# Kernel optimization log

Measured on AMD Instinct MI355X. Metric: run time of the kernel, lower is better.

Reference implementation:

```python
import jax, jax.numpy as jnp
import numpy as np

DT = 0.05
DX = 1.0
NUM_STEPS = 3
EPS = 1e-6
MAX_COEFF = 1.0  # use_implicit=True


def _thomas_const(r, d, eps):
    """Batched Thomas solve for the constant-coefficient system used by the ADI
    sweeps: off-diagonals a=c=-r, diagonal 1+2r with Neumann-like ends 1+r.
    Faithful to the torch solver including the +eps on b[0] and the
    clamp(min=eps) on interior denominators. d: (M, n) -> (M, n)."""
    n = d.shape[-1]
    a = -r  # scalar (lower == upper == -r)
    b = jnp.full((n,), 1.0 + 2.0 * r, dtype=d.dtype).at[0].set(1.0 + r).at[-1].set(1.0 + r)
    # forward elimination for c' and denominators (scalar per position)
    cp0 = a / (b[0] + eps)
    def fwd_c(cp_prev, bi):
        denom = jnp.maximum(bi - a * cp_prev, eps)
        cp = a / denom
        return cp, (cp, denom)
    _, (cps, denoms) = jax.lax.scan(fwd_c, cp0, b[1:])
    cp = jnp.concatenate([cp0[None], cps]).at[-1].set(0.0)  # (n,); last entry unused (torch leaves it 0)
    # forward sweep for d' over the whole batch of RHS vectors
    dT = jnp.moveaxis(d, -1, 0)  # (n, M)
    dp0 = dT[0] / (b[0] + eps)
    def fwd_d(dp_prev, xs):
        di, denom = xs
        dp = (di - a * dp_prev) / denom
        return dp, dp
    _, dps = jax.lax.scan(fwd_d, dp0, (dT[1:], denoms))
    dp = jnp.concatenate([dp0[None], dps], axis=0)  # (n, M)
    # back substitution
    xn = dp[-1]
    def back(x_next, xs):
        dpi, cpi = xs
        x = dpi - cpi * x_next
        return x, x
    _, xs_ = jax.lax.scan(back, xn, (dp[:-1], cp[:-1]), reverse=True)
    x = jnp.concatenate([xs_, xn[None]], axis=0)  # (n, M)
    return jnp.moveaxis(x, 0, -1)


def _forward(u, alpha_base, beta_base, alpha_spatial, beta_spatial, channel_coupling):
    B, C, H, W = u.shape
    # torch.einsum('cc,bci->bci', coupling, u) multiplies by the DIAGONAL of coupling
    diag = jnp.diagonal(channel_coupling)  # (C,)
    for step in range(NUM_STEPS):
        t = step * DT
        alpha_t = jnp.clip(alpha_base + alpha_spatial.mean(axis=(1, 2)) * t, EPS, MAX_COEFF)  # (C,)
        beta_t = jnp.clip(beta_base + beta_spatial.mean(axis=(1, 2)) * t, EPS, MAX_COEFF)
        r_a = alpha_t * (DT / 2.0) / DX ** 2  # ADI half-steps
        r_b = beta_t * (DT / 2.0) / DX ** 2
        uc = jnp.moveaxis(u, 1, 0)  # (C, B, H, W); coefficients differ per channel
        solve_x = lambda r, d: _thomas_const(r, d.reshape(B * H, W), EPS).reshape(B, H, W)
        ux = jax.vmap(solve_x)(r_a, uc)
        solve_y = lambda r, d: jnp.swapaxes(
            _thomas_const(r, jnp.swapaxes(d, 1, 2).reshape(B * W, H), EPS).reshape(B, W, H), 1, 2)
        uy = jax.vmap(solve_y)(r_b, ux)
        u = jnp.moveaxis(uy, 0, 1) * diag[None, :, None, None]
    return u


def setup_inputs() -> dict:
    key = jax.random.key(0)
    k = jax.random.split(key, 6)
    B, C, S = 128, 3, 256
    u = jax.random.normal(k[0], (B, C, S, S), dtype=jnp.float32)
    alpha_base = 0.3 + 0.01 * jax.random.normal(k[1], (C,), dtype=jnp.float32)
    beta_base = 0.3 + 0.01 * jax.random.normal(k[2], (C,), dtype=jnp.float32)
    alpha_spatial = 0.01 * jax.random.normal(k[3], (C, S, S), dtype=jnp.float32)
    beta_spatial = 0.01 * jax.random.normal(k[4], (C, S, S), dtype=jnp.float32)
    channel_coupling = 0.05 * jnp.eye(C, dtype=jnp.float32) + 0.01 * jax.random.normal(k[5], (C, C), dtype=jnp.float32)
    return {"u": u, "alpha_base": alpha_base, "beta_base": beta_base,
            "alpha_spatial": alpha_spatial, "beta_spatial": beta_spatial,
            "channel_coupling": channel_coupling}


def reference(u, alpha_base, beta_base, alpha_spatial, beta_spatial, channel_coupling):
    return _forward(u, alpha_base, beta_base, alpha_spatial, beta_spatial, channel_coupling)
```

## Files before the change

kernel.cpp:

```cpp
#include <hip/hip_runtime.h>

constexpr int Bn = 128, Cn = 3, Sn = 256;
constexpr int HWn = Sn * Sn;
constexpr int NPLANE = Bn * Cn;
constexpr float DTf = 0.05f;
constexpr float EPSf = 1e-6f;
constexpr float MAXCf = 1.0f;

#define WS_TAPX 128
#define WS_TAPY 10368

__global__ void build_taps(const float* __restrict__ alpha_base,
                           const float* __restrict__ beta_base,
                           const float* __restrict__ aspat,
                           const float* __restrict__ bspat,
                           const float* __restrict__ coupling,
                           float* __restrict__ ws) {
  __shared__ double sm[256];
  __shared__ float cp3[3][288], di3[3][288];
  __shared__ float s_mean;
  const int dirc = blockIdx.x, dir = dirc / 3, c = dirc % 3;
  const int j = threadIdx.x;
  {
    const float4* p = (const float4*)((dir == 0 ? aspat : bspat) + c * HWn) + j;
    double acc = 0.0;
#pragma unroll
    for (int k2 = 0; k2 < 64; ++k2) {
      float4 v = p[k2 * 256];
      acc += (double)v.x + (double)v.y + (double)v.z + (double)v.w;
    }
    sm[j] = acc;
    __syncthreads();
    for (int s2 = 128; s2 > 0; s2 >>= 1) {
      if (j < s2) sm[j] += sm[j + s2];
      __syncthreads();
    }
    if (j == 0) s_mean = (float)(sm[0] * (1.0 / 65536.0));
    __syncthreads();
  }
  if (j < 3) {
    const int k = j;
    const float base = (dir == 0) ? alpha_base[c] : beta_base[c];
    const float coef = fminf(fmaxf(base + s_mean * ((float)k * DTf), EPSf), MAXCf);
    const float r = coef * (DTf * 0.5f);
    for (int p = 0; p < 16; ++p) {
      cp3[k][p] = 0.f; di3[k][p] = 0.f;
      cp3[k][272 + p] = 0.f; di3[k][272 + p] = 0.f;
    }
    float b0 = 1.f + r + EPSf;
    float cq = -r / b0, dq = 1.f / b0;
    cp3[k][16] = cq; di3[k][16] = dq;
    for (int i = 1; i < 256; ++i) {
      float b = (i == 255) ? (1.f + r) : (1.f + 2.f * r);
      float den = fmaxf(b + r * cq, EPSf);
      cq = -r / den; dq = 1.f / den;
      cp3[k][16 + i] = cq; di3[k][16 + i] = dq;
    }
  }
  float* tb = ws + ((dir == 0) ? WS_TAPX : WS_TAPY) + c * 13 * 256;
#pragma unroll
  for (int d = 0; d < 13; ++d) tb[d * 256 + j] = 0.f;
  __syncthreads();

  float z[33];
#pragma unroll
  for (int o = 0; o < 33; ++o) z[o] = (o == 16) ? 1.f : 0.f;
#pragma unroll
  for (int k = 0; k < 3; ++k) {
    float dp = 0.f;
#pragma unroll
    for (int o = 0; o < 33; ++o) {
      const int p = j + o;
      dp = fmaf(-cp3[k][p], dp, z[o] * di3[k][p]);
      z[o] = dp;
    }
    float x = 0.f;
#pragma unroll
    for (int o = 32; o >= 0; --o) {
      const int p = j + o;
      x = fmaf(-cp3[k][p], x, z[o]);
      z[o] = x;
    }
  }
  float scale = 1.f;
  if (dir == 1) {
    float dgc = coupling[c * 3 + c];
    scale = dgc * dgc * dgc;
  }
#pragma unroll
  for (int o = -6; o <= 6; ++o) {
    const int i = j + o;
    if ((unsigned)i < 256u) tb[(6 - o) * 256 + i] = z[o + 16] * scale;
  }
}

__global__ __launch_bounds__(512, 4) void conv3(
    const float* __restrict__ src, float* __restrict__ dst,
    const float* __restrict__ ws) {
  __shared__ float vt[76 * 256];
  const int t = threadIdx.x;
  const int logical = (blockIdx.x & 7) * 192 + (blockIdx.x >> 3);
  const int plane = logical >> 2;
  const int st = logical & 3;
  const int c = plane % 3;
  const int h0 = st * 64;
  const int a = (st == 0) ? 0 : (h0 - 6);
  const int b = (st == 3) ? 256 : (h0 + 70);
  const int Wv = b - a;
  const float* tpx = ws + WS_TAPX + c * 3328;
  const float* tpy = ws + WS_TAPY + c * 3328;
  const float* srcp = src + (size_t)plane * HWn;

  {
    const int wv = t >> 6, l = t & 63;
    const int fl = l ^ (l >> 3);
#pragma unroll
    for (int m = 0; m < 3; ++m) {
#pragma unroll
      for (int jj = 0; jj < 4; ++jj) {
        const int rl = 4 * wv + jj + 32 * m;
        if (rl < Wv) {
          const float* gp = srcp + (size_t)(a + rl) * 256 + (fl << 2);
          __builtin_amdgcn_global_load_lds(
              (const __attribute__((address_space(1))) void*)gp,
              (__attribute__((address_space(3))) void*)(vt + rl * 256), 16, 0, 0);
        }
      }
    }
  }
  float tx[13];
#pragma unroll
  for (int d = 0; d < 13; ++d) tx[d] = tpx[d * 256 + 128];
  asm volatile("s_waitcnt vmcnt(0)" ::: "memory");
  __builtin_amdgcn_sched_barrier(0);

  const int NU = 16 * Wv;
#pragma unroll
  for (int p = 0; p < 3; ++p) {
    const int u = t + 512 * p;
    if (u < NU) {
      const int s = u & 15, rl = u >> 4;
      float* base = vt + rl * 256;
      float in_[32];
#pragma unroll
      for (int mq = 0; mq < 8; ++mq) {
        int g = 4 * s - 2 + mq;
        g = g < 0 ? 0 : (g > 63 ? 63 : g);
        const int sl = g ^ (g >> 3);
        *(float4*)&in_[4 * mq] = *(const float4*)(base + 4 * sl);
      }
      float acc[16];
#pragma unroll
      for (int e = 0; e < 16; ++e) acc[e] = tx[0] * in_[e + 2];
#pragma unroll
      for (int d = 1; d < 13; ++d)
#pragma unroll
        for (int e = 0; e < 16; ++e) acc[e] = fmaf(tx[d], in_[e + 2 + d], acc[e]);
      if (s == 0) {
#pragma unroll
        for (int e = 0; e < 6; ++e) {
          float ac = 0.f;
#pragma unroll
          for (int d = 0; d < 13; ++d) ac = fmaf(tpx[d * 256 + e], in_[e + 2 + d], ac);
          acc[e] = ac;
        }
      } else if (s == 15) {
#pragma unroll
        for (int e = 10; e < 16; ++e) {
          float ac = 0.f;
#pragma unroll
          for (int d = 0; d < 13; ++d) ac = fmaf(tpx[d * 256 + 240 + e], in_[e + 2 + d], ac);
          acc[e] = ac;
        }
      }
#pragma unroll
      for (int jj = 0; jj < 4; ++jj) {
        const int q = 4 * s + jj;
        const int sl = q ^ (q >> 3);
        *(float4*)(base + 4 * sl) =
            make_float4(acc[4 * jj], acc[4 * jj + 1], acc[4 * jj + 2], acc[4 * jj + 3]);
      }
    }
  }
  __syncthreads();

  const int pr = t & 127, rc = t >> 7;
  const int jq = pr >> 1;
  const int wpos = ((jq ^ (jq >> 3)) << 2) | ((pr & 1) * 2);
  const int g0 = h0 + 16 * rc;
  float2 win[13];
#pragma unroll
  for (int m = 0; m < 12; ++m) {
    int gg = g0 - 6 + m;
    gg = gg < a ? a : gg;
    win[m] = *(const float2*)(vt + (gg - a) * 256 + wpos);
  }
  float* dstp = dst + (size_t)plane * HWn + 2 * pr;
#pragma unroll
  for (int rr = 0; rr < 16; ++rr) {
    const int g = g0 + rr;
    {
      int gg = g + 6;
      gg = gg > b - 1 ? b - 1 : gg;
      win[12] = *(const float2*)(vt + (gg - a) * 256 + wpos);
    }
    const int gu = __builtin_amdgcn_readfirstlane(g);
    float ox, oy;
    {
      const float ty = tpy[gu];
      ox = ty * win[0].x; oy = ty * win[0].y;
    }
#pragma unroll
    for (int d = 1; d < 13; ++d) {
      const float ty = tpy[d * 256 + gu];
      ox = fmaf(ty, win[d].x, ox);
      oy = fmaf(ty, win[d].y, oy);
    }
    *(float2*)(dstp + (size_t)g * 256) = make_float2(ox, oy);
#pragma unroll
    for (int m = 0; m < 12; ++m) win[m] = win[m + 1];
  }
}

extern "C" void kernel_launch(void* const* d_in, const int* in_sizes, int n_in,
                              void* d_out, int out_size, void* d_ws, size_t ws_size,
                              hipStream_t stream) {
  const float* u = (const float*)d_in[0];
  const float* alpha_base = (const float*)d_in[1];
  const float* beta_base = (const float*)d_in[2];
  const float* alpha_spatial = (const float*)d_in[3];
  const float* beta_spatial = (const float*)d_in[4];
  const float* coupling = (const float*)d_in[5];
  float* out = (float*)d_out;
  float* ws = (float*)d_ws;

  build_taps<<<6, 256, 0, stream>>>(alpha_base, beta_base,
                                    alpha_spatial, beta_spatial, coupling, ws);
  conv3<<<NPLANE * 4, 512, 0, stream>>>(u, out, ws);
}
```

Before: 90.69 us.

## Stream row chunks through small LDS ring buffer pipelining x and y stencils

Replaces the load-all-then-compute conv kernel with an 11-iteration loop. Each iteration loads 8 rows into a small staging buffer, applies the x-direction stencil into a 32-row ring buffer, and computes y-direction outputs from earlier rows. The aim is to cut LDS use from 76 rows to 40 so occupancy can rise (launch bounds 4→6) and to overlap global loads with compute. In exchange it adds two barriers per iteration, a full vmcnt wait each step, and padded rows whose float4 accesses may be misaligned.

```diff
diff --git a/kernel.cpp b/kernel.cpp
--- a/kernel.cpp
+++ b/kernel.cpp
@@ -94,131 +94,120 @@
   }
 }
 
-__global__ __launch_bounds__(512, 4) void conv3(
+__global__ __launch_bounds__(512, 6) void conv_pipe(
     const float* __restrict__ src, float* __restrict__ dst,
     const float* __restrict__ ws) {
-  __shared__ float vt[76 * 256];
+  __shared__ float Vb[32 * 266];
+  __shared__ float Ub[8 * 266];
   const int t = threadIdx.x;
   const int logical = (blockIdx.x & 7) * 192 + (blockIdx.x >> 3);
   const int plane = logical >> 2;
-  const int st = logical & 3;
+  const int R = logical & 3;
   const int c = plane % 3;
-  const int h0 = st * 64;
-  const int a = (st == 0) ? 0 : (h0 - 6);
-  const int b = (st == 3) ? 256 : (h0 + 70);
-  const int Wv = b - a;
   const float* tpx = ws + WS_TAPX + c * 3328;
   const float* tpy = ws + WS_TAPY + c * 3328;
   const float* srcp = src + (size_t)plane * HWn;
-
-  {
-    const int wv = t >> 6, l = t & 63;
-    const int fl = l ^ (l >> 3);
-#pragma unroll
-    for (int m = 0; m < 3; ++m) {
-#pragma unroll
-      for (int jj = 0; jj < 4; ++jj) {
-        const int rl = 4 * wv + jj + 32 * m;
-        if (rl < Wv) {
-          const float* gp = srcp + (size_t)(a + rl) * 256 + (fl << 2);
-          __builtin_amdgcn_global_load_lds(
-              (const __attribute__((address_space(1))) void*)gp,
-              (__attribute__((address_space(3))) void*)(vt + rl * 256), 16, 0, 0);
+  float* dstp = dst + (size_t)plane * HWn;
+  const int g_base = 64 * R - 6;
+
+  float tx[13];
+#pragma unroll
+  for (int d = 0; d < 13; ++d) tx[d] = tpx[d * 256 + 128];
+
+  const int xs = t >> 3, xr = t & 7;
+  const int yp = t & 127, ysub = t >> 7;
+  const int wv = t >> 6, l = t & 63;
+
+  for (int i = 0; i < 11; ++i) {
+    if (i < 10) {
+      const int r = 8 * i + wv;
+      if (r < 76) {
+        int G = g_base + r;
+        G = G < 0 ? 0 : (G > 255 ? 255 : G);
+        const float* gp = srcp + (size_t)G * 256 + 4 * l;
+        __builtin_amdgcn_global_load_lds(
+            (const __attribute__((address_space(1))) void*)gp,
+            (__attribute__((address_space(3))) void*)(Ub + wv * 266), 16, 0, 0);
+      }
+    }
+    if (i >= 3) {
+      const int j = i - 3;
+      const int r0 = 6 + 8 * j + 2 * ysub;
+      const int g0 = g_base + r0;
+      float2 win[14];
+#pragma unroll
+      for (int d = 0; d < 14; ++d) {
+        const int slot = (r0 - 6 + d) & 31;
+        win[d] = *(const float2*)(Vb + slot * 266 + 2 * yp);
+      }
+      const int gu = __builtin_amdgcn_readfirstlane(g0);
+      float ox0, oy0, ox1, oy1;
+      {
+        const float ty0 = tpy[gu];
+        ox0 = ty0 * win[0].x; oy0 = ty0 * win[0].y;
+        const float ty1 = tpy[gu + 1];
+        ox1 = ty1 * win[1].x; oy1 = ty1 * win[1].y;
+      }
+#pragma unroll
+      for (int d = 1; d < 13; ++d) {
+        const float ty0 = tpy[d * 256 + gu];
+        ox0 = fmaf(ty0, win[d].x, ox0); oy0 = fmaf(ty0, win[d].y, oy0);
+        const float ty1 = tpy[d * 256 + gu + 1];
+        ox1 = fmaf(ty1, win[d + 1].x, ox1); oy1 = fmaf(ty1, win[d + 1].y, oy1);
+      }
+      *(float2*)(dstp + (size_t)g0 * 256 + 2 * yp) = make_float2(ox0, oy0);
+      *(float2*)(dstp + (size_t)(g0 + 1) * 256 + 2 * yp) = make_float2(ox1, oy1);
+    }
+    asm volatile("s_waitcnt vmcnt(0)" ::: "memory");
+    __syncthreads();
+    if (i < 10) {
+      const int r = 8 * i + xr;
+      if (r < 76) {
+        float in_[16];
+#pragma unroll
+        for (int m = 0; m < 8; ++m) {
+          int cp = 4 * xs - 6 + 2 * m;
+          cp = cp < 0 ? 0 : (cp > 254 ? 254 : cp);
+          *(float2*)&in_[2 * m] = *(const float2*)(Ub + xr * 266 + cp);
         }
-      }
-    }
-  }
-  float tx[13];
-#pragma unroll
-  for (int d = 0; d < 13; ++d) tx[d] = tpx[d * 256 + 128];
-  asm volatile("s_waitcnt vmcnt(0)" ::: "memory");
-  __builtin_amdgcn_sched_barrier(0);
-
-  const int NU = 16 * Wv;
-#pragma unroll
-  for (int p = 0; p < 3; ++p) {
-    const int u = t + 512 * p;
-    if (u < NU) {
-      const int s = u & 15, rl = u >> 4;
-      float* base = vt + rl * 256;
-      float in_[32];
-#pragma unroll
-      for (int mq = 0; mq < 8; ++mq) {
-        int g = 4 * s - 2 + mq;
-        g = g < 0 ? 0 : (g > 63 ? 63 : g);
-        const int sl = g ^ (g >> 3);
-        *(float4*)&in_[4 * mq] = *(const float4*)(base + 4 * sl);
-      }
-      float acc[16];
-#pragma unroll
-      for (int e = 0; e < 16; ++e) acc[e] = tx[0] * in_[e + 2];
-#pragma unroll
-      for (int d = 1; d < 13; ++d)
-#pragma unroll
-        for (int e = 0; e < 16; ++e) acc[e] = fmaf(tx[d], in_[e + 2 + d], acc[e]);
-      if (s == 0) {
-#pragma unroll
-        for (int e = 0; e < 6; ++e) {
-          float ac = 0.f;
-#pragma unroll
-          for (int d = 0; d < 13; ++d) ac = fmaf(tpx[d * 256 + e], in_[e + 2 + d], ac);
-          acc[e] = ac;
+        float acc[4];
+#pragma unroll
+        for (int e = 0; e < 4; ++e) acc[e] = tx[0] * in_[e];
+#pragma unroll
+        for (int d = 1; d < 13; ++d)
+#pragma unroll
+          for (int e = 0; e < 4; ++e) acc[e] = fmaf(tx[d], in_[e + d], acc[e]);
+        if (xs < 2) {
+#pragma unroll
+          for (int e = 0; e < 4; ++e) {
+            const int col = 4 * xs + e;
+            if (col < 6) {
+              float a = 0.f;
+#pragma unroll
+              for (int d = 0; d < 13; ++d)
+                a = fmaf(tpx[d * 256 + col], in_[e + d], a);
+              acc[e] = a;
+            }
+          }
+        } else if (xs >= 62) {
+#pragma unroll
+          for (int e = 0; e < 4; ++e) {
+            const int col = 4 * xs + e;
+            if (col >= 250) {
+              float a = 0.f;
+#pragma unroll
+              for (int d = 0; d < 13; ++d)
+                a = fmaf(tpx[d * 256 + col], in_[e + d], a);
+              acc[e] = a;
+            }
+          }
         }
-      } else if (s == 15) {
-#pragma unroll
-        for (int e = 10; e < 16; ++e) {
-          float ac = 0.f;
-#pragma unroll
-          for (int d = 0; d < 13; ++d) ac = fmaf(tpx[d * 256 + 240 + e], in_[e + 2 + d], ac);
-          acc[e] = ac;
-        }
-      }
-#pragma unroll
-      for (int jj = 0; jj < 4; ++jj) {
-        const int q = 4 * s + jj;
-        const int sl = q ^ (q >> 3);
-        *(float4*)(base + 4 * sl) =
-            make_float4(acc[4 * jj], acc[4 * jj + 1], acc[4 * jj + 2], acc[4 * jj + 3]);
-      }
-    }
-  }
-  __syncthreads();
-
-  const int pr = t & 127, rc = t >> 7;
-  const int jq = pr >> 1;
-  const int wpos = ((jq ^ (jq >> 3)) << 2) | ((pr & 1) * 2);
-  const int g0 = h0 + 16 * rc;
-  float2 win[13];
-#pragma unroll
-  for (int m = 0; m < 12; ++m) {
-    int gg = g0 - 6 + m;
-    gg = gg < a ? a : gg;
-    win[m] = *(const float2*)(vt + (gg - a) * 256 + wpos);
-  }
-  float* dstp = dst + (size_t)plane * HWn + 2 * pr;
-#pragma unroll
-  for (int rr = 0; rr < 16; ++rr) {
-    const int g = g0 + rr;
-    {
-      int gg = g + 6;
-      gg = gg > b - 1 ? b - 1 : gg;
-      win[12] = *(const float2*)(vt + (gg - a) * 256 + wpos);
-    }
-    const int gu = __builtin_amdgcn_readfirstlane(g);
-    float ox, oy;
-    {
-      const float ty = tpy[gu];
-      ox = ty * win[0].x; oy = ty * win[0].y;
-    }
-#pragma unroll
-    for (int d = 1; d < 13; ++d) {
-      const float ty = tpy[d * 256 + gu];
-      ox = fmaf(ty, win[d].x, ox);
-      oy = fmaf(ty, win[d].y, oy);
-    }
-    *(float2*)(dstp + (size_t)g * 256) = make_float2(ox, oy);
-#pragma unroll
-    for (int m = 0; m < 12; ++m) win[m] = win[m + 1];
+        const int slot = r & 31;
+        *(float4*)(Vb + slot * 266 + 4 * xs) =
+            make_float4(acc[0], acc[1], acc[2], acc[3]);
+      }
+    }
+    __syncthreads();
   }
 }
 
@@ -236,5 +225,5 @@
 
   build_taps<<<6, 256, 0, stream>>>(alpha_base, beta_base,
                                     alpha_spatial, beta_spatial, coupling, ws);
-  conv3<<<NPLANE * 4, 512, 0, stream>>>(u, out, ws);
+  conv_pipe<<<NPLANE * 4, 512, 0, stream>>>(u, out, ws);
 }
```

Measured after the change: 238.9 us. 163% more time.

## Split fused separable convolution into separate x and y kernels via workspace

Applied to the files above, without the earlier changes.

Replaces the single fused conv3 kernel with two kernels: convx applies the horizontal 13-tap filter row-wise and writes to a full-size workspace buffer, and convy applies the vertical filter from that buffer. This removes the halo recomputation and large LDS footprint of the fused tile but adds a full extra write and read of the 100MB intermediate. The fallback conv3 now reads global memory directly instead of using async LDS loads, and uses a different LDS swizzle. Which path runs depends on the workspace size.

```diff
diff --git a/kernel.cpp b/kernel.cpp
--- a/kernel.cpp
+++ b/kernel.cpp
@@ -9,6 +9,7 @@
 
 #define WS_TAPX 128
 #define WS_TAPY 10368
+#define WS_TMP  20480
 
 __global__ void build_taps(const float* __restrict__ alpha_base,
                            const float* __restrict__ beta_base,
@@ -91,6 +92,101 @@
   for (int o = -6; o <= 6; ++o) {
     const int i = j + o;
     if ((unsigned)i < 256u) tb[(6 - o) * 256 + i] = z[o + 16] * scale;
+  }
+}
+
+__global__ __launch_bounds__(256, 4) void convx(
+    const float* __restrict__ src, float* __restrict__ tmp,
+    const float* __restrict__ ws) {
+  const int t = threadIdx.x;
+  const int rid = blockIdx.x * 16 + (t >> 4);
+  const int s = t & 15;
+  const int c = (rid >> 8) % 3;
+  const float* tpx = ws + WS_TAPX + c * 3328;
+  float tx[13];
+#pragma unroll
+  for (int d = 0; d < 13; ++d) tx[d] = tpx[d * 256 + 128];
+  const float* row = src + (size_t)rid * 256;
+  float in_[32];
+#pragma unroll
+  for (int mq = 0; mq < 8; ++mq) {
+    int cl = 16 * s - 8 + 4 * mq;
+    cl = cl < 0 ? 0 : (cl > 252 ? 252 : cl);
+    *(float4*)&in_[4 * mq] = *(const float4*)(row + cl);
+  }
+  float acc[16];
+#pragma unroll
+  for (int e = 0; e < 16; ++e) acc[e] = tx[0] * in_[e + 2];
+#pragma unroll
+  for (int d = 1; d < 13; ++d)
+#pragma unroll
+    for (int e = 0; e < 16; ++e) acc[e] = fmaf(tx[d], in_[e + 2 + d], acc[e]);
+  if (s == 0) {
+#pragma unroll
+    for (int e = 0; e < 6; ++e) {
+      float ac = 0.f;
+#pragma unroll
+      for (int d = 0; d < 13; ++d) ac = fmaf(tpx[d * 256 + e], in_[e + 2 + d], ac);
+      acc[e] = ac;
+    }
+  } else if (s == 15) {
+#pragma unroll
+    for (int e = 10; e < 16; ++e) {
+      float ac = 0.f;
+#pragma unroll
+      for (int d = 0; d < 13; ++d) ac = fmaf(tpx[d * 256 + 240 + e], in_[e + 2 + d], ac);
+      acc[e] = ac;
+    }
+  }
+  float* op = tmp + (size_t)rid * 256 + 16 * s;
+#pragma unroll
+  for (int jj = 0; jj < 4; ++jj)
+    *(float4*)(op + 4 * jj) =
+        make_float4(acc[4 * jj], acc[4 * jj + 1], acc[4 * jj + 2], acc[4 * jj + 3]);
+}
+
+__global__ __launch_bounds__(256, 4) void convy(
+    const float* __restrict__ tmp, float* __restrict__ dst,
+    const float* __restrict__ ws) {
+  const int t = threadIdx.x;
+  const int plane = blockIdx.x >> 2;
+  const int chunk = (blockIdx.x & 3) * 2 + (t >> 7);
+  const int pair = t & 127;
+  const int c = plane % 3;
+  const float* tpy = ws + WS_TAPY + c * 3328;
+  const float* tp = tmp + (size_t)plane * HWn + 2 * pair;
+  float* dp = dst + (size_t)plane * HWn + 2 * pair;
+  const int g0 = 32 * chunk;
+  float2 win[13];
+#pragma unroll
+  for (int m = 0; m < 12; ++m) {
+    int gg = g0 - 6 + m;
+    gg = gg < 0 ? 0 : gg;
+    win[m] = *(const float2*)(tp + (size_t)gg * 256);
+  }
+#pragma unroll
+  for (int rr = 0; rr < 32; ++rr) {
+    const int g = g0 + rr;
+    {
+      int gg = g + 6;
+      gg = gg > 255 ? 255 : gg;
+      win[12] = *(const float2*)(tp + (size_t)gg * 256);
+    }
+    const int gu = __builtin_amdgcn_readfirstlane(g);
+    float ox, oy;
+    {
+      const float ty = tpy[gu];
+      ox = ty * win[0].x; oy = ty * win[0].y;
+    }
+#pragma unroll
+    for (int d = 1; d < 13; ++d) {
+      const float ty = tpy[d * 256 + gu];
+      ox = fmaf(ty, win[d].x, ox);
+      oy = fmaf(ty, win[d].y, oy);
+    }
+    *(float2*)(dp + (size_t)g * 256) = make_float2(ox, oy);
+#pragma unroll
+    for (int m = 0; m < 12; ++m) win[m] = win[m + 1];
   }
 }
 
@@ -109,30 +205,10 @@
   const int Wv = b - a;
   const float* tpx = ws + WS_TAPX + c * 3328;
   const float* tpy = ws + WS_TAPY + c * 3328;
+  float tx[13];
+#pragma unroll
+  for (int d = 0; d < 13; ++d) tx[d] = tpx[d * 256 + 128];
   const float* srcp = src + (size_t)plane * HWn;
-
-  {
-    const int wv = t >> 6, l = t & 63;
-    const int fl = l ^ (l >> 3);
-#pragma unroll
-    for (int m = 0; m < 3; ++m) {
-#pragma unroll
-      for (int jj = 0; jj < 4; ++jj) {
-        const int rl = 4 * wv + jj + 32 * m;
-        if (rl < Wv) {
-          const float* gp = srcp + (size_t)(a + rl) * 256 + (fl << 2);
-          __builtin_amdgcn_global_load_lds(
-              (const __attribute__((address_space(1))) void*)gp,
-              (__attribute__((address_space(3))) void*)(vt + rl * 256), 16, 0, 0);
-        }
-      }
-    }
-  }
-  float tx[13];
-#pragma unroll
-  for (int d = 0; d < 13; ++d) tx[d] = tpx[d * 256 + 128];
-  asm volatile("s_waitcnt vmcnt(0)" ::: "memory");
-  __builtin_amdgcn_sched_barrier(0);
 
   const int NU = 16 * Wv;
 #pragma unroll
@@ -140,14 +216,13 @@
     const int u = t + 512 * p;
     if (u < NU) {
       const int s = u & 15, rl = u >> 4;
-      float* base = vt + rl * 256;
+      const float* row = srcp + (size_t)(a + rl) * 256;
       float in_[32];
 #pragma unroll
       for (int mq = 0; mq < 8; ++mq) {
-        int g = 4 * s - 2 + mq;
-        g = g < 0 ? 0 : (g > 63 ? 63 : g);
-        const int sl = g ^ (g >> 3);
-        *(float4*)&in_[4 * mq] = *(const float4*)(base + 4 * sl);
+        int cl = 16 * s - 8 + 4 * mq;
+        cl = cl < 0 ? 0 : (cl > 252 ? 252 : cl);
+        *(float4*)&in_[4 * mq] = *(const float4*)(row + cl);
       }
       float acc[16];
 #pragma unroll
@@ -173,27 +248,26 @@
           acc[e] = ac;
         }
       }
-#pragma unroll
-      for (int jj = 0; jj < 4; ++jj) {
-        const int q = 4 * s + jj;
-        const int sl = q ^ (q >> 3);
-        *(float4*)(base + 4 * sl) =
+      const int sw = rl & 7;
+      float4* vr = (float4*)vt + rl * 64;
+#pragma unroll
+      for (int jj = 0; jj < 4; ++jj)
+        vr[(4 * s + jj) ^ sw] =
             make_float4(acc[4 * jj], acc[4 * jj + 1], acc[4 * jj + 2], acc[4 * jj + 3]);
-      }
     }
   }
   __syncthreads();
 
   const int pr = t & 127, rc = t >> 7;
-  const int jq = pr >> 1;
-  const int wpos = ((jq ^ (jq >> 3)) << 2) | ((pr & 1) * 2);
+  const int jq = pr >> 1, jin = (pr & 1) * 2;
   const int g0 = h0 + 16 * rc;
   float2 win[13];
 #pragma unroll
   for (int m = 0; m < 12; ++m) {
     int gg = g0 - 6 + m;
     gg = gg < a ? a : gg;
-    win[m] = *(const float2*)(vt + (gg - a) * 256 + wpos);
+    const int rl = gg - a;
+    win[m] = *(const float2*)(vt + rl * 256 + (((jq ^ (rl & 7)) << 2) | jin));
   }
   float* dstp = dst + (size_t)plane * HWn + 2 * pr;
 #pragma unroll
@@ -202,7 +276,8 @@
     {
       int gg = g + 6;
       gg = gg > b - 1 ? b - 1 : gg;
-      win[12] = *(const float2*)(vt + (gg - a) * 256 + wpos);
+      const int rl = gg - a;
+      win[12] = *(const float2*)(vt + rl * 256 + (((jq ^ (rl & 7)) << 2) | jin));
     }
     const int gu = __builtin_amdgcn_readfirstlane(g);
     float ox, oy;
@@ -236,5 +311,12 @@
 
   build_taps<<<6, 256, 0, stream>>>(alpha_base, beta_base,
                                     alpha_spatial, beta_spatial, coupling, ws);
-  conv3<<<NPLANE * 4, 512, 0, stream>>>(u, out, ws);
-}
+  const size_t need = (size_t)(WS_TMP + (size_t)NPLANE * HWn) * sizeof(float);
+  if (ws_size >= need) {
+    float* tmp = ws + WS_TMP;
+    convx<<<NPLANE * 16, 256, 0, stream>>>(u, tmp, ws);
+    convy<<<NPLANE * 4, 256, 0, stream>>>(tmp, out, ws);
+  } else {
+    conv3<<<NPLANE * 4, 512, 0, stream>>>(u, out, ws);
+  }
+}
```

Measured after the change: 170.9 us. 88.5% more time.

## Double-buffer row chunks in LDS to overlap loads with separable convolution

Applied to the files above, without the earlier changes.

Each block now covers half a plane instead of a quarter. It walks that half in five 26-row chunks, using two LDS buffers so the async global-to-LDS load of the next chunk overlaps the horizontal and vertical tap passes on the current one. The intent is to hide global load latency that the old single-shot load exposed before any compute could start. In exchange, each chunk reloads a 12-row halo, which raises read traffic, and the grid is half as large. The vertical pass also stores scalar floats instead of float2, and a hand-tuned vmcnt wait now governs buffer reuse.

```diff
diff --git a/kernel.cpp b/kernel.cpp
--- a/kernel.cpp
+++ b/kernel.cpp
@@ -94,131 +94,160 @@
   }
 }
 
-__global__ __launch_bounds__(512, 4) void conv3(
+__global__ __launch_bounds__(512, 4) void conv_pipe(
     const float* __restrict__ src, float* __restrict__ dst,
     const float* __restrict__ ws) {
-  __shared__ float vt[76 * 256];
+  __shared__ float vt[2][38 * 256];
   const int t = threadIdx.x;
-  const int logical = (blockIdx.x & 7) * 192 + (blockIdx.x >> 3);
-  const int plane = logical >> 2;
-  const int st = logical & 3;
+  const int logical = (blockIdx.x & 7) * 96 + (blockIdx.x >> 3);
+  const int plane = logical >> 1;
+  const int h = logical & 1;
   const int c = plane % 3;
-  const int h0 = st * 64;
-  const int a = (st == 0) ? 0 : (h0 - 6);
-  const int b = (st == 3) ? 256 : (h0 + 70);
-  const int Wv = b - a;
   const float* tpx = ws + WS_TAPX + c * 3328;
   const float* tpy = ws + WS_TAPY + c * 3328;
   const float* srcp = src + (size_t)plane * HWn;
+  float* dstp = dst + (size_t)plane * HWn;
+
+  float tx[13];
+#pragma unroll
+  for (int d = 0; d < 13; ++d) tx[d] = tpx[d * 256 + 128];
+
+  const int wv = t >> 6, l = t & 63;
+  const int fl = l ^ (l >> 3);
 
   {
-    const int wv = t >> 6, l = t & 63;
-    const int fl = l ^ (l >> 3);
-#pragma unroll
-    for (int m = 0; m < 3; ++m) {
-#pragma unroll
-      for (int jj = 0; jj < 4; ++jj) {
-        const int rl = 4 * wv + jj + 32 * m;
-        if (rl < Wv) {
-          const float* gp = srcp + (size_t)(a + rl) * 256 + (fl << 2);
-          __builtin_amdgcn_global_load_lds(
-              (const __attribute__((address_space(1))) void*)gp,
-              (__attribute__((address_space(3))) void*)(vt + rl * 256), 16, 0, 0);
+    const int c0 = 130 * h;
+    const int aa = (c0 - 6 < 0) ? 0 : (c0 - 6);
+    const int W = ((c0 + 32 > 256) ? 256 : (c0 + 32)) - aa;
+#pragma unroll
+    for (int m = 0; m < 5; ++m) {
+      int rl = wv + 8 * m;
+      if (rl > W - 1) rl = W - 1;
+      const float* gp = srcp + (size_t)(aa + rl) * 256 + (fl << 2);
+      __builtin_amdgcn_global_load_lds(
+          (const __attribute__((address_space(1))) void*)gp,
+          (__attribute__((address_space(3))) void*)(&vt[0][0] + rl * 256), 16, 0, 0);
+    }
+  }
+  asm volatile("s_waitcnt vmcnt(0)" ::: "memory");
+  __builtin_amdgcn_s_barrier();
+  __builtin_amdgcn_sched_barrier(0);
+
+  for (int s = 0; s < 5; ++s) {
+    const int cur = s & 1;
+    const int c0 = 130 * h + 26 * s;
+    const int c1 = (h == 1 && s == 4) ? 256 : (c0 + 26);
+    const int aa = (c0 - 6 < 0) ? 0 : (c0 - 6);
+    const int bb = (c0 + 32 > 256) ? 256 : (c0 + 32);
+    const int W = bb - aa;
+    float* vb = &vt[cur][0];
+
+    if (s < 4) {
+      const int nc0 = c0 + 26;
+      const int naa = nc0 - 6;
+      const int nW = ((nc0 + 32 > 256) ? 256 : (nc0 + 32)) - naa;
+      float* nb = &vt[cur ^ 1][0];
+#pragma unroll
+      for (int m = 0; m < 5; ++m) {
+        int rl = wv + 8 * m;
+        if (rl > nW - 1) rl = nW - 1;
+        const float* gp = srcp + (size_t)(naa + rl) * 256 + (fl << 2);
+        __builtin_amdgcn_global_load_lds(
+            (const __attribute__((address_space(1))) void*)gp,
+            (__attribute__((address_space(3))) void*)(nb + rl * 256), 16, 0, 0);
+      }
+    }
+
+    {
+      const int NU = 16 * W;
+#pragma unroll
+      for (int p = 0; p < 2; ++p) {
+        const int u = t + 512 * p;
+        if (u < NU) {
+          const int sg = u & 15, rl = u >> 4;
+          float* rowl = vb + rl * 256;
+          float in_[32];
+#pragma unroll
+          for (int mm = 0; mm < 8; ++mm) {
+            int q = 4 * sg - 2 + mm;
+            q = q < 0 ? 0 : (q > 63 ? 63 : q);
+            const int sl = q ^ (q >> 3);
+            *(float4*)&in_[4 * mm] = *(const float4*)(rowl + 4 * sl);
+          }
+          float acc[16];
+#pragma unroll
+          for (int e = 0; e < 16; ++e) acc[e] = tx[0] * in_[e + 2];
+#pragma unroll
+          for (int d = 1; d < 13; ++d)
+#pragma unroll
+            for (int e = 0; e < 16; ++e) acc[e] = fmaf(tx[d], in_[e + 2 + d], acc[e]);
+          if (sg == 0) {
+#pragma unroll
+            for (int e = 0; e < 6; ++e) {
+              float ac = 0.f;
+#pragma unroll
+              for (int d = 0; d < 13; ++d)
+                ac = fmaf(tpx[d * 256 + e], in_[e + 2 + d], ac);
+              acc[e] = ac;
+            }
+          } else if (sg == 15) {
+#pragma unroll
+            for (int e = 10; e < 16; ++e) {
+              float ac = 0.f;
+#pragma unroll
+              for (int d = 0; d < 13; ++d)
+                ac = fmaf(tpx[d * 256 + 240 + e], in_[e + 2 + d], ac);
+              acc[e] = ac;
+            }
+          }
+#pragma unroll
+          for (int jj = 0; jj < 4; ++jj) {
+            const int q = 4 * sg + jj;
+            const int sl = q ^ (q >> 3);
+            *(float4*)(rowl + 4 * sl) =
+                make_float4(acc[4 * jj], acc[4 * jj + 1], acc[4 * jj + 2], acc[4 * jj + 3]);
+          }
         }
       }
     }
-  }
-  float tx[13];
-#pragma unroll
-  for (int d = 0; d < 13; ++d) tx[d] = tpx[d * 256 + 128];
-  asm volatile("s_waitcnt vmcnt(0)" ::: "memory");
-  __builtin_amdgcn_sched_barrier(0);
-
-  const int NU = 16 * Wv;
-#pragma unroll
-  for (int p = 0; p < 3; ++p) {
-    const int u = t + 512 * p;
-    if (u < NU) {
-      const int s = u & 15, rl = u >> 4;
-      float* base = vt + rl * 256;
-      float in_[32];
-#pragma unroll
-      for (int mq = 0; mq < 8; ++mq) {
-        int g = 4 * s - 2 + mq;
-        g = g < 0 ? 0 : (g > 63 ? 63 : g);
-        const int sl = g ^ (g >> 3);
-        *(float4*)&in_[4 * mq] = *(const float4*)(base + 4 * sl);
-      }
-      float acc[16];
-#pragma unroll
-      for (int e = 0; e < 16; ++e) acc[e] = tx[0] * in_[e + 2];
-#pragma unroll
-      for (int d = 1; d < 13; ++d)
-#pragma unroll
-        for (int e = 0; e < 16; ++e) acc[e] = fmaf(tx[d], in_[e + 2 + d], acc[e]);
-      if (s == 0) {
-#pragma unroll
-        for (int e = 0; e < 6; ++e) {
-          float ac = 0.f;
-#pragma unroll
-          for (int d = 0; d < 13; ++d) ac = fmaf(tpx[d * 256 + e], in_[e + 2 + d], ac);
-          acc[e] = ac;
+    asm volatile("s_waitcnt lgkmcnt(0)" ::: "memory");
+    __builtin_amdgcn_s_barrier();
+    __builtin_amdgcn_sched_barrier(0);
+
+    {
+      const int j = t & 255, rc2 = t >> 8;
+      const int jq = j >> 2;
+      const int wpos = ((jq ^ (jq >> 3)) << 2) | (j & 3);
+      const int g0 = c0 + 13 * rc2;
+      const int gend = (c1 < g0 + 13) ? c1 : (g0 + 13);
+      float win[13];
+#pragma unroll
+      for (int m = 0; m < 12; ++m) {
+        int gg = g0 - 6 + m;
+        gg = gg < aa ? aa : gg;
+        win[m] = vb[(gg - aa) * 256 + wpos];
+      }
+      float* dcol = dstp + j;
+#pragma unroll
+      for (int rr = 0; rr < 13; ++rr) {
+        const int g = g0 + rr;
+        if (g < gend) {
+          int gg = g + 6;
+          gg = gg > bb - 1 ? bb - 1 : gg;
+          win[12] = vb[(gg - aa) * 256 + wpos];
+          const int gu = __builtin_amdgcn_readfirstlane(g);
+          float o = tpy[gu] * win[0];
+#pragma unroll
+          for (int d = 1; d < 13; ++d) o = fmaf(tpy[d * 256 + gu], win[d], o);
+          dcol[(size_t)g * 256] = o;
+#pragma unroll
+          for (int m = 0; m < 12; ++m) win[m] = win[m + 1];
         }
-      } else if (s == 15) {
-#pragma unroll
-        for (int e = 10; e < 16; ++e) {
-          float ac = 0.f;
-#pragma unroll
-          for (int d = 0; d < 13; ++d) ac = fmaf(tpx[d * 256 + 240 + e], in_[e + 2 + d], ac);
-          acc[e] = ac;
-        }
-      }
-#pragma unroll
-      for (int jj = 0; jj < 4; ++jj) {
-        const int q = 4 * s + jj;
-        const int sl = q ^ (q >> 3);
-        *(float4*)(base + 4 * sl) =
-            make_float4(acc[4 * jj], acc[4 * jj + 1], acc[4 * jj + 2], acc[4 * jj + 3]);
-      }
-    }
-  }
-  __syncthreads();
-
-  const int pr = t & 127, rc = t >> 7;
-  const int jq = pr >> 1;
-  const int wpos = ((jq ^ (jq >> 3)) << 2) | ((pr & 1) * 2);
-  const int g0 = h0 + 16 * rc;
-  float2 win[13];
-#pragma unroll
-  for (int m = 0; m < 12; ++m) {
-    int gg = g0 - 6 + m;
-    gg = gg < a ? a : gg;
-    win[m] = *(const float2*)(vt + (gg - a) * 256 + wpos);
-  }
-  float* dstp = dst + (size_t)plane * HWn + 2 * pr;
-#pragma unroll
-  for (int rr = 0; rr < 16; ++rr) {
-    const int g = g0 + rr;
-    {
-      int gg = g + 6;
-      gg = gg > b - 1 ? b - 1 : gg;
-      win[12] = *(const float2*)(vt + (gg - a) * 256 + wpos);
-    }
-    const int gu = __builtin_amdgcn_readfirstlane(g);
-    float ox, oy;
-    {
-      const float ty = tpy[gu];
-      ox = ty * win[0].x; oy = ty * win[0].y;
-    }
-#pragma unroll
-    for (int d = 1; d < 13; ++d) {
-      const float ty = tpy[d * 256 + gu];
-      ox = fmaf(ty, win[d].x, ox);
-      oy = fmaf(ty, win[d].y, oy);
-    }
-    *(float2*)(dstp + (size_t)g * 256) = make_float2(ox, oy);
-#pragma unroll
-    for (int m = 0; m < 12; ++m) win[m] = win[m + 1];
+      }
+    }
+    asm volatile("s_waitcnt vmcnt(13) lgkmcnt(0)" ::: "memory");
+    __builtin_amdgcn_s_barrier();
+    __builtin_amdgcn_sched_barrier(0);
   }
 }
 
@@ -236,5 +265,5 @@
 
   build_taps<<<6, 256, 0, stream>>>(alpha_base, beta_base,
                                     alpha_spatial, beta_spatial, coupling, ws);
-  conv3<<<NPLANE * 4, 512, 0, stream>>>(u, out, ws);
+  conv_pipe<<<NPLANE * 2, 512, 0, stream>>>(u, out, ws);
 }
```

Measured after the change: 115.4 us. 27.2% more time.
